# Kernel tuning notes

Measured on AMD Instinct MI355X. Metric: run time of the kernel, lower is better.

## Reference

```python
import jax, jax.numpy as jnp
import numpy as np

D = 100  # input_size


def _gru_scan(x, h0, wi, wh, bi, bh):
    # x: [B,T,Din], h0: [B,H], wi: [3H,Din], wh: [3H,H]  (PyTorch r,z,n gate order)
    xw = jnp.einsum('btd,gd->btg', x, wi) + bi  # [B,T,3H]
    def step(h, xt):
        gh = h @ wh.T + bh
        xr, xz, xn = jnp.split(xt, 3, axis=-1)
        hr, hz, hn = jnp.split(gh, 3, axis=-1)
        r = jax.nn.sigmoid(xr + hr)
        z = jax.nn.sigmoid(xz + hz)
        n = jnp.tanh(xn + r * hn)
        hn2 = (1 - z) * n + z * h
        return hn2, hn2
    _, ys = jax.lax.scan(step, h0, jnp.swapaxes(xw, 0, 1))
    return jnp.swapaxes(ys, 0, 1)  # [B,T,H]


def _bigru(x, wi, wh, bi, bh):
    B = x.shape[0]
    H = wh.shape[-1]
    h0 = jnp.zeros((B, H), x.dtype)
    f = _gru_scan(x, h0, wi[0], wh[0], bi[0], bh[0])
    b = _gru_scan(x[:, ::-1], h0, wi[1], wh[1], bi[1], bh[1])[:, ::-1]
    return jnp.concatenate([f, b], axis=-1)


def _gru_cell(x, h, wi, wh, bi, bh):
    gx = x @ wi.T + bi
    gh = h @ wh.T + bh
    xr, xz, xn = jnp.split(gx, 3, axis=-1)
    hr, hz, hn = jnp.split(gh, 3, axis=-1)
    r = jax.nn.sigmoid(xr + hr)
    z = jax.nn.sigmoid(xz + hz)
    n = jnp.tanh(xn + r * hn)
    return (1 - z) * n + z * h


def setup_inputs() -> dict:
    key = jax.random.key(0)
    ks = iter(jax.random.split(key, 40))
    def n(shape, s=0.08):
        return (jax.random.normal(next(ks), shape) * s).astype(jnp.float32)
    B, T, L, V = 32, 512, 64, 400000
    inp = {
        'x_word': jax.random.randint(next(ks), (B, T), 0, V),
        'x_query': jax.random.randint(next(ks), (B, L), 0, V),
        'embed': n((V, D), 0.3),
        'ctx_wi': n((2, 3 * D, D)), 'ctx_wh': n((2, 3 * D, D)),
        'ctx_bi': n((2, 3 * D)), 'ctx_bh': n((2, 3 * D)),
        'mod0_wi': n((2, 3 * D, 8 * D)), 'mod0_wh': n((2, 3 * D, D)),
        'mod0_bi': n((2, 3 * D)), 'mod0_bh': n((2, 3 * D)),
        'mod1_wi': n((2, 3 * D, 2 * D)), 'mod1_wh': n((2, 3 * D, D)),
        'mod1_bi': n((2, 3 * D)), 'mod1_bh': n((2, 3 * D)),
        'w_sim': n((6 * D,)),
        'enc_wi': n((12 * D, 2 * D)), 'enc_wh': n((12 * D, 4 * D)),
        'enc_bi': n((12 * D,)), 'enc_bh': n((12 * D,)),
        'dec_wi': n((12 * D, 2 * D)), 'dec_wh': n((12 * D, 4 * D)),
        'dec_bi': n((12 * D,)), 'dec_bh': n((12 * D,)),
        'w1': n((2 * D, 4 * D)), 'w2': n((2 * D, 4 * D)), 'vt': n((2 * D,)),
    }
    return inp


def reference(x_word, x_query, embed, ctx_wi, ctx_wh, ctx_bi, ctx_bh,
              mod0_wi, mod0_wh, mod0_bi, mod0_bh, mod1_wi, mod1_wh, mod1_bi, mod1_bh,
              w_sim, enc_wi, enc_wh, enc_bi, enc_bh, dec_wi, dec_wh, dec_bi, dec_bh,
              w1, w2, vt):
    B, T = x_word.shape
    # shared bidirectional context encoder over both context and query
    h = _bigru(embed[x_word], ctx_wi, ctx_wh, ctx_bi, ctx_bh)   # [B,T,2D]
    u = _bigru(embed[x_query], ctx_wi, ctx_wh, ctx_bi, ctx_bh)  # [B,L,2D]
    # trilinear similarity W @ cat(h,u,h*u), fused (no [B,T,L,6D] materialization)
    w1s, w2s, w3s = jnp.split(w_sim, 3)
    S = (jnp.einsum('btd,d->bt', h, w1s)[:, :, None]
         + jnp.einsum('bld,d->bl', u, w2s)[:, None, :]
         + jnp.einsum('btd,bld->btl', h * w3s, u))               # [B,T,L]
    c2q = jnp.einsum('btl,bld->btd', jax.nn.softmax(S, axis=-1), u)
    b_att = jax.nn.softmax(jnp.max(S, axis=2), axis=-1)          # [B,T]
    q2c = jnp.einsum('bt,btd->bd', b_att, h)[:, None, :]         # [B,1,2D]
    G = jnp.concatenate([h, c2q, h * c2q, h * q2c], axis=-1)     # [B,T,8D]
    # 2-layer bidirectional modeling GRU
    M = _bigru(G, mod0_wi, mod0_wh, mod0_bi, mod0_bh)
    M = _bigru(M, mod1_wi, mod1_wh, mod1_bi, mod1_bh)            # [B,T,2D]
    # pointer network
    enc = _gru_scan(M, jnp.zeros((B, 4 * D), M.dtype), enc_wi, enc_wh, enc_bi, enc_bh)  # [B,T,4D]
    enc_w1 = jnp.einsum('bth,ph->btp', enc, w1)                  # precompute W1 @ enc
    hid = jnp.zeros((B, 4 * D), M.dtype)
    dec_in = jnp.zeros((B, 2 * D), M.dtype)  # never updated (as in original)
    probs = []
    for _ in range(2):  # answers = 2 (start, end)
        hid = _gru_cell(dec_in, hid, dec_wi, dec_wh, dec_bi, dec_bh)
        blend = jnp.tanh(enc_w1 + (hid @ w2.T)[:, None, :])      # [B,T,2D]
        out = jnp.einsum('btp,p->bt', blend, vt)
        probs.append(jax.nn.log_softmax(out, axis=-1))
    return jnp.stack(probs, axis=1)  # [B,2,T]
```

## Files before the change

kernel.cpp:

```cpp
#include <hip/hip_runtime.h>
#include <hip/hip_bf16.h>

typedef __hip_bfloat16 bf16;
typedef unsigned long long u64;
typedef __attribute__((ext_vector_type(8))) short s8v;
typedef __attribute__((ext_vector_type(4))) short s4v;
typedef __attribute__((ext_vector_type(4))) float f4v;

#define DEV __device__ __forceinline__

DEV float to_f32(float x) { return x; }
DEV float to_f32(bf16 x) { return __bfloat162float(x); }
DEV void store_c(float* p, float v) { *p = v; }
DEV void store_c(bf16* p, float v) { *p = __float2bfloat16(v); }
DEV float sigmf(float x) { return 1.f / (1.f + __expf(-x)); }

__global__ void gather_embed_bf(const int* __restrict__ idx, const float* __restrict__ embed,
                                bf16* __restrict__ out, int ntok) {
  int i = blockIdx.x * blockDim.x + threadIdx.x;
  if (i >= ntok * 100) return;
  int t = i / 100;
  int d = i - t * 100;
  out[i] = __float2bfloat16(embed[(size_t)idx[t] * 100 + d]);
}

__global__ void cvt_bf16(const float* __restrict__ in, bf16* __restrict__ out, int n) {
  int i = blockIdx.x * blockDim.x + threadIdx.x;
  if (i < n) out[i] = __float2bfloat16(in[i]);
}

template <typename TC, bool HAS_BIAS>
__global__ __launch_bounds__(256) void gemm_mfma(
    const bf16* __restrict__ A, const bf16* __restrict__ W,
    const float* __restrict__ bias, TC* __restrict__ C,
    int M, int N, int K) {
  __shared__ short Als[128 * 32];
  __shared__ short Wls[64 * 32];
  const int tid = threadIdx.x;
  const int m0 = blockIdx.x * 128;
  const int n0 = blockIdx.y * 64;
  const int lane = tid & 63;
  const int wv = tid >> 6;
  const int wm = wv >> 1, wn = wv & 1;
  const int lq = lane >> 4, lr = lane & 15;
  const int arow = tid >> 1;
  const int ah = tid & 1;
  const int wrow = (tid & 127) >> 1;

  f4v acc[4][2];
#pragma unroll
  for (int i = 0; i < 4; ++i)
#pragma unroll
    for (int j = 0; j < 2; ++j) acc[i][j] = (f4v){0.f, 0.f, 0.f, 0.f};

  for (int k0 = 0; k0 < K; k0 += 32) {
#pragma unroll
    for (int ss = 0; ss < 2; ++ss) {
      int s = 2 * ah + ss;
      int kk = k0 + s * 8;
      short* dst = &Als[arow * 32 + s * 8];
      const short* src = (const short*)(A + (size_t)(m0 + arow) * K + kk);
      if (kk + 8 <= K) {
        *(s4v*)dst = *(const s4v*)src;
        *(s4v*)(dst + 4) = *(const s4v*)(src + 4);
      } else {
#pragma unroll
        for (int j = 0; j < 8; ++j) dst[j] = (kk + j < K) ? src[j] : (short)0;
      }
    }
    if (tid < 128) {
      int nrow = n0 + wrow;
#pragma unroll
      for (int ss = 0; ss < 2; ++ss) {
        int s = 2 * (tid & 1) + ss;
        int kk = k0 + s * 8;
        short* dst = &Wls[wrow * 32 + s * 8];
        if (nrow < N) {
          const short* src = (const short*)(W + (size_t)nrow * K + kk);
          if (kk + 8 <= K) {
            *(s4v*)dst = *(const s4v*)src;
            *(s4v*)(dst + 4) = *(const s4v*)(src + 4);
          } else {
#pragma unroll
            for (int j = 0; j < 8; ++j) dst[j] = (kk + j < K) ? src[j] : (short)0;
          }
        } else {
#pragma unroll
          for (int j = 0; j < 8; ++j) dst[j] = (short)0;
        }
      }
    }
    __syncthreads();
    s8v af[4], bfr[2];
#pragma unroll
    for (int mi = 0; mi < 4; ++mi) {
      int r = wm * 64 + mi * 16 + lr;
      af[mi] = *(const s8v*)&Als[r * 32 + lq * 8];
    }
#pragma unroll
    for (int ni = 0; ni < 2; ++ni) {
      int r = wn * 32 + ni * 16 + lr;
      bfr[ni] = *(const s8v*)&Wls[r * 32 + lq * 8];
    }
#pragma unroll
    for (int mi = 0; mi < 4; ++mi)
#pragma unroll
      for (int ni = 0; ni < 2; ++ni)
        acc[mi][ni] = __builtin_amdgcn_mfma_f32_16x16x32_bf16(af[mi], bfr[ni], acc[mi][ni], 0, 0, 0);
    __syncthreads();
  }
#pragma unroll
  for (int mi = 0; mi < 4; ++mi) {
#pragma unroll
    for (int ni = 0; ni < 2; ++ni) {
      int n = n0 + wn * 32 + ni * 16 + lr;
      if (n >= N) continue;
      float bv = HAS_BIAS ? bias[n] : 0.f;
#pragma unroll
      for (int r = 0; r < 4; ++r) {
        int m = m0 + wm * 64 + mi * 16 + lq * 4 + r;
        store_c(&C[(size_t)m * N + n], acc[mi][ni][r] + bv);
      }
    }
  }
}

template <typename TO>
__global__ __launch_bounds__(320) void gru_scan100_reg(
    const bf16* __restrict__ xw_f, const bf16* __restrict__ xw_b,
    const float* __restrict__ wh,
    const float* __restrict__ bh,
    TO* __restrict__ out,
    int T) {
  const int b = blockIdx.x, dir = blockIdx.y;
  const bf16* xw = dir ? xw_b : xw_f;
  __shared__ float h_s[100];
  __shared__ float g_s[300];
  const int tid = threadIdx.x;
  float w[100];
  float bias = 0.f;
  if (tid < 300) {
    const float* wrow = wh + (size_t)dir * 30000 + (size_t)tid * 100;
#pragma unroll
    for (int c = 0; c < 25; ++c) {
      float4 v = *(const float4*)(wrow + 4 * c);
      w[4 * c] = v.x; w[4 * c + 1] = v.y; w[4 * c + 2] = v.z; w[4 * c + 3] = v.w;
    }
    bias = bh[dir * 300 + tid];
  }
  if (tid < 100) h_s[tid] = 0.f;
  __syncthreads();
  for (int step = 0; step < T; ++step) {
    int t = dir ? (T - 1 - step) : step;
    if (tid < 300) {
      float a0 = bias, a1 = 0.f, a2 = 0.f, a3 = 0.f;
#pragma unroll
      for (int c = 0; c < 25; ++c) {
        float4 h4 = *(const float4*)(&h_s[4 * c]);
        a0 += w[4 * c] * h4.x; a1 += w[4 * c + 1] * h4.y;
        a2 += w[4 * c + 2] * h4.z; a3 += w[4 * c + 3] * h4.w;
      }
      g_s[tid] = (a0 + a1) + (a2 + a3);
    }
    __syncthreads();
    if (tid < 100) {
      size_t base = ((size_t)b * T + t) * 300;
      float xr = to_f32(xw[base + tid]);
      float xz = to_f32(xw[base + 100 + tid]);
      float xn = to_f32(xw[base + 200 + tid]);
      float rr = sigmf(xr + g_s[tid]);
      float zz = sigmf(xz + g_s[100 + tid]);
      float nn = tanhf(xn + rr * g_s[200 + tid]);
      float hn = (1.f - zz) * nn + zz * h_s[tid];
      h_s[tid] = hn;
      store_c(&out[((size_t)b * T + t) * 200 + dir * 100 + tid], hn);
    }
    __syncthreads();
  }
}

__global__ __launch_bounds__(640) void gru_scan_enc_tag(
    const bf16* __restrict__ xw,
    const float* __restrict__ wh,
    const float* __restrict__ bh,
    bf16* __restrict__ out,
    u64* __restrict__ hx,
    int T) {
  const int b = blockIdx.x, s = blockIdx.y;
  __shared__ float h_s[400];
  __shared__ float g_s[150];
  const int tid = threadIdx.x;
  const int g = tid >> 2, p = tid & 3;
  const bool active = (tid < 600);
  float w[100];
  float bias = 0.f;
  if (active) {
    int i = g % 50, grp = g / 50;
    int gidx = grp * 400 + s * 50 + i;
    const float* wrow = wh + (size_t)gidx * 400 + p * 100;
#pragma unroll
    for (int c = 0; c < 25; ++c) {
      float4 v = *(const float4*)(wrow + 4 * c);
      w[4 * c] = v.x; w[4 * c + 1] = v.y; w[4 * c + 2] = v.z; w[4 * c + 3] = v.w;
    }
    if (p == 0) bias = bh[gidx];
  }
  for (int k = tid; k < 400; k += 640) h_s[k] = 0.f;
  const int myi = s * 50 + tid;
  float pxr = 0.f, pxz = 0.f, pxn = 0.f;
  if (tid < 50) {
    size_t base0 = (size_t)b * T * 1200;
    pxr = to_f32(xw[base0 + myi]);
    pxz = to_f32(xw[base0 + 400 + myi]);
    pxn = to_f32(xw[base0 + 800 + myi]);
  }
  __syncthreads();

  for (int t = 0; t < T; ++t) {
    if (active) {
      float a0 = bias, a1 = 0.f, a2 = 0.f, a3 = 0.f;
      const int hb = p * 100;
#pragma unroll
      for (int c = 0; c < 25; ++c) {
        float4 h4 = *(const float4*)(&h_s[hb + 4 * c]);
        a0 += w[4 * c] * h4.x; a1 += w[4 * c + 1] * h4.y;
        a2 += w[4 * c + 2] * h4.z; a3 += w[4 * c + 3] * h4.w;
      }
      float acc = (a0 + a1) + (a2 + a3);
      acc += __shfl_xor(acc, 1);
      acc += __shfl_xor(acc, 2);
      if (p == 0) g_s[g] = acc;
    }
    __syncthreads();
    const int par = (t + 1) & 1;
    u64* hxp = hx + ((size_t)b * 2 + par) * 400;
    if (tid < 50) {
      float rr = sigmf(pxr + g_s[tid]);
      float zz = sigmf(pxz + g_s[50 + tid]);
      float nn = tanhf(pxn + rr * g_s[100 + tid]);
      float hn = (1.f - zz) * nn + zz * h_s[myi];
      out[((size_t)b * T + t) * 400 + myi] = __float2bfloat16(hn);
      h_s[myi] = hn;
      u64 pack = (u64)__float_as_uint(hn) | ((u64)(unsigned)(t + 1) << 32);
      __hip_atomic_store(&hxp[myi], pack, __ATOMIC_RELAXED, __HIP_MEMORY_SCOPE_AGENT);
      if (t + 1 < T) {
        size_t basen = ((size_t)b * T + (t + 1)) * 1200;
        pxr = to_f32(xw[basen + myi]);
        pxz = to_f32(xw[basen + 400 + myi]);
        pxn = to_f32(xw[basen + 800 + myi]);
      }
    }
    if (tid < 400 && (tid / 50) != s) {
      const u64* src = &hxp[tid];
      u64 v;
      for (;;) {
        v = __hip_atomic_load(src, __ATOMIC_RELAXED, __HIP_MEMORY_SCOPE_AGENT);
        if ((unsigned)(v >> 32) == (unsigned)(t + 1)) break;
        __builtin_amdgcn_s_sleep(1);
      }
      h_s[tid] = __uint_as_float((unsigned)v);
    }
    __syncthreads();
  }
}

__global__ __launch_bounds__(64) void rowdot200(const float* __restrict__ X, const float* __restrict__ w,
                                                float* __restrict__ out, int rows) {
  int r = blockIdx.x;
  int lane = threadIdx.x;
  const float* x = X + (size_t)r * 200;
  float s = x[lane] * w[lane] + x[lane + 64] * w[lane + 64] + x[lane + 128] * w[lane + 128];
  if (lane < 8) s += x[lane + 192] * w[lane + 192];
  for (int off = 32; off; off >>= 1) s += __shfl_down(s, off);
  if (lane == 0) out[r] = s;
}

__global__ __launch_bounds__(256) void attn_main(
    const float* __restrict__ h,
    const float* __restrict__ u,
    const float* __restrict__ th,
    const float* __restrict__ tu,
    const float* __restrict__ w_sim,
    float* __restrict__ c2q,
    float* __restrict__ smax,
    int T) {
  const int b = blockIdx.x;
  const int t0 = blockIdx.y * 32;
  __shared__ float u_s[64 * 201];
  __shared__ float tu_s[64];
  __shared__ float w3_s[200];
  __shared__ float hw3_s[200];
  __shared__ float Sp[4][64];
  __shared__ float A_s[64];
  const int tid = threadIdx.x;
  for (int i = tid; i < 64 * 200; i += 256) {
    int l = i / 200, d = i - l * 200;
    u_s[l * 201 + d] = u[((size_t)b * 64 + l) * 200 + d];
  }
  if (tid < 64) tu_s[tid] = tu[b * 64 + tid];
  if (tid < 200) w3_s[tid] = w_sim[400 + tid];
  __syncthreads();
  for (int tt = 0; tt < 32; ++tt) {
    int t = t0 + tt;
    if (tid < 200) hw3_s[tid] = h[((size_t)b * T + t) * 200 + tid] * w3_s[tid];
    __syncthreads();
    int l = tid & 63, q = tid >> 6;
    float p = 0.f;
    for (int d = q * 50; d < q * 50 + 50; ++d) p += hw3_s[d] * u_s[l * 201 + d];
    Sp[q][l] = p;
    __syncthreads();
    if (tid < 64) {
      float s = th[b * T + t] + tu_s[l] + Sp[0][l] + Sp[1][l] + Sp[2][l] + Sp[3][l];
      float m = s;
      for (int off = 32; off; off >>= 1) m = fmaxf(m, __shfl_xor(m, off));
      float e = __expf(s - m);
      float ssum = e;
      for (int off = 32; off; off >>= 1) ssum += __shfl_xor(ssum, off);
      A_s[l] = e / ssum;
      if (l == 0) smax[b * T + t] = m;
    }
    __syncthreads();
    if (tid < 200) {
      float acc = 0.f;
      for (int l2 = 0; l2 < 64; ++l2) acc += A_s[l2] * u_s[l2 * 201 + tid];
      c2q[((size_t)b * T + t) * 200 + tid] = acc;
    }
    __syncthreads();
  }
}

__global__ __launch_bounds__(256) void softmax_T(const float* __restrict__ in, float* __restrict__ outv, int T) {
  int b = blockIdx.x;
  int tid = threadIdx.x;
  __shared__ float red[256];
  float m = -1e30f;
  for (int t = tid; t < T; t += 256) m = fmaxf(m, in[b * T + t]);
  red[tid] = m;
  __syncthreads();
  for (int s = 128; s; s >>= 1) {
    if (tid < s) red[tid] = fmaxf(red[tid], red[tid + s]);
    __syncthreads();
  }
  m = red[0];
  __syncthreads();
  float sum = 0.f;
  for (int t = tid; t < T; t += 256) sum += __expf(in[b * T + t] - m);
  red[tid] = sum;
  __syncthreads();
  for (int s = 128; s; s >>= 1) {
    if (tid < s) red[tid] += red[tid + s];
    __syncthreads();
  }
  float inv = 1.f / red[0];
  for (int t = tid; t < T; t += 256) outv[b * T + t] = __expf(in[b * T + t] - m) * inv;
}

__global__ __launch_bounds__(256) void q2c_kernel(const float* __restrict__ batt, const float* __restrict__ h,
                                                  float* __restrict__ q2c, int T) {
  int b = blockIdx.x;
  int tid = threadIdx.x;
  if (tid < 200) {
    float acc = 0.f;
    for (int t = 0; t < T; ++t) acc += batt[b * T + t] * h[((size_t)b * T + t) * 200 + tid];
    q2c[b * 200 + tid] = acc;
  }
}

__global__ void build_G(const float* __restrict__ h, const float* __restrict__ c2q,
                        const float* __restrict__ q2c, bf16* __restrict__ G, int T) {
  size_t i = (size_t)blockIdx.x * blockDim.x + threadIdx.x;
  if (i >= (size_t)32 * T * 200) return;
  size_t row = i / 200;
  int d = (int)(i - row * 200);
  int b = (int)(row / T);
  float hv = h[i];
  float cv = c2q[i];
  float qv = q2c[b * 200 + d];
  bf16* g = G + row * 800;
  g[d] = __float2bfloat16(hv);
  g[200 + d] = __float2bfloat16(cv);
  g[400 + d] = __float2bfloat16(hv * cv);
  g[600 + d] = __float2bfloat16(hv * qv);
}

__global__ __launch_bounds__(512) void decoder_small(
    const float* __restrict__ dwh,
    const float* __restrict__ dbi, const float* __restrict__ dbh,
    const float* __restrict__ w2,
    float* __restrict__ d2out) {
  __shared__ float hid[400];
  __shared__ float hid2[400];
  __shared__ float gh[1200];
  const int tid = threadIdx.x;
  if (tid < 400) {
    float r = sigmf(dbi[tid] + dbh[tid]);
    float z = sigmf(dbi[400 + tid] + dbh[400 + tid]);
    float n = tanhf(dbi[800 + tid] + r * dbh[800 + tid]);
    hid[tid] = (1.f - z) * n;
  }
  __syncthreads();
  if (tid < 200) {
    float a = 0.f;
    for (int k = 0; k < 400; ++k) a += w2[(size_t)tid * 400 + k] * hid[k];
    d2out[tid] = a;
  }
  for (int j = tid; j < 1200; j += 512) {
    float a = dbh[j];
    for (int k = 0; k < 400; ++k) a += dwh[(size_t)j * 400 + k] * hid[k];
    gh[j] = a;
  }
  __syncthreads();
  if (tid < 400) {
    float r = sigmf(dbi[tid] + gh[tid]);
    float z = sigmf(dbi[400 + tid] + gh[400 + tid]);
    float n = tanhf(dbi[800 + tid] + r * gh[800 + tid]);
    hid2[tid] = (1.f - z) * n + z * hid[tid];
  }
  __syncthreads();
  if (tid < 200) {
    float a = 0.f;
    for (int k = 0; k < 400; ++k) a += w2[(size_t)tid * 400 + k] * hid2[k];
    d2out[200 + tid] = a;
  }
}

__global__ __launch_bounds__(64) void logits_kernel(
    const float* __restrict__ encw1,
    const float* __restrict__ d2,
    const float* __restrict__ vt,
    float* __restrict__ outp,
    int T) {
  int row = blockIdx.x;
  int b = row / T, t = row - b * T;
  int lane = threadIdx.x;
  const float* e = encw1 + (size_t)row * 200;
  float s0 = 0.f, s1 = 0.f;
  for (int p = lane; p < 200; p += 64) {
    float ev = e[p], v = vt[p];
    s0 += tanhf(ev + d2[p]) * v;
    s1 += tanhf(ev + d2[200 + p]) * v;
  }
  for (int off = 32; off; off >>= 1) {
    s0 += __shfl_down(s0, off);
    s1 += __shfl_down(s1, off);
  }
  if (lane == 0) {
    outp[((size_t)b * 2 + 0) * T + t] = s0;
    outp[((size_t)b * 2 + 1) * T + t] = s1;
  }
}

__global__ __launch_bounds__(256) void log_softmax_T(float* __restrict__ x, int T) {
  int row = blockIdx.x;
  float* p = x + (size_t)row * T;
  __shared__ float red[256];
  int tid = threadIdx.x;
  float m = -1e30f;
  for (int t = tid; t < T; t += 256) m = fmaxf(m, p[t]);
  red[tid] = m;
  __syncthreads();
  for (int s = 128; s; s >>= 1) {
    if (tid < s) red[tid] = fmaxf(red[tid], red[tid + s]);
    __syncthreads();
  }
  m = red[0];
  __syncthreads();
  float sum = 0.f;
  for (int t = tid; t < T; t += 256) sum += __expf(p[t] - m);
  red[tid] = sum;
  __syncthreads();
  for (int s = 128; s; s >>= 1) {
    if (tid < s) red[tid] += red[tid + s];
    __syncthreads();
  }
  float lse = m + __logf(red[0]);
  __syncthreads();
  for (int t = tid; t < T; t += 256) p[t] = p[t] - lse;
}

extern "C" void kernel_launch(void* const* d_in, const int* in_sizes, int n_in,
                              void* d_out, int out_size, void* d_ws, size_t ws_size,
                              hipStream_t stream) {
  (void)in_sizes; (void)n_in; (void)out_size; (void)ws_size;
  const int B = 32, T = 512, L = 64;
  const int BT = B * T;
  const int BL = B * L;

  const int* x_word = (const int*)d_in[0];
  const int* x_query = (const int*)d_in[1];
  const float* embed = (const float*)d_in[2];
  const float* ctx_wi = (const float*)d_in[3];
  const float* ctx_wh = (const float*)d_in[4];
  const float* ctx_bi = (const float*)d_in[5];
  const float* ctx_bh = (const float*)d_in[6];
  const float* mod0_wi = (const float*)d_in[7];
  const float* mod0_wh = (const float*)d_in[8];
  const float* mod0_bi = (const float*)d_in[9];
  const float* mod0_bh = (const float*)d_in[10];
  const float* mod1_wi = (const float*)d_in[11];
  const float* mod1_wh = (const float*)d_in[12];
  const float* mod1_bi = (const float*)d_in[13];
  const float* mod1_bh = (const float*)d_in[14];
  const float* w_sim = (const float*)d_in[15];
  const float* enc_wi = (const float*)d_in[16];
  const float* enc_wh = (const float*)d_in[17];
  const float* enc_bi = (const float*)d_in[18];
  const float* enc_bh = (const float*)d_in[19];
  const float* dec_wh = (const float*)d_in[21];
  const float* dec_bi = (const float*)d_in[22];
  const float* dec_bh = (const float*)d_in[23];
  const float* w1 = (const float*)d_in[24];
  const float* w2 = (const float*)d_in[25];
  const float* vt = (const float*)d_in[26];
  float* out_f = (float*)d_out;

  char* ws = (char*)d_ws;
  size_t off = 0;
  auto alloc = [&](size_t bytes) -> void* {
    void* p = ws + off;
    off += (bytes + 255) & ~(size_t)255;
    return p;
  };
  u64* hx = (u64*)alloc((size_t)B * 2 * 400 * 8);
  bf16* ewbf = (bf16*)alloc((size_t)BT * 100 * 2);
  bf16* eqbf = (bf16*)alloc((size_t)BL * 100 * 2);
  bf16* ctx_wibf = (bf16*)alloc((size_t)60000 * 2);
  bf16* mod0_wibf = (bf16*)alloc((size_t)480000 * 2);
  bf16* mod1_wibf = (bf16*)alloc((size_t)120000 * 2);
  bf16* enc_wibf = (bf16*)alloc((size_t)240000 * 2);
  bf16* w1bf = (bf16*)alloc((size_t)80000 * 2);
  char* RA = (char*)alloc((size_t)BT * 1200 * 2);
  bf16* xwA = (bf16*)RA;
  bf16* xwB = (bf16*)(RA + (size_t)BT * 300 * 2);
  bf16* xwe = (bf16*)RA;
  bf16* xwqF = (bf16*)alloc((size_t)BL * 300 * 2);
  bf16* xwqB = (bf16*)alloc((size_t)BL * 300 * 2);
  char* RB = (char*)alloc((size_t)BT * 800 * 2);
  bf16* G = (bf16*)RB;
  bf16* enc_outbf = (bf16*)RB;
  char* RC = (char*)alloc((size_t)2 * BT * 200 * 4);
  float* h_cat = (float*)RC;
  float* c2q = (float*)(RC + (size_t)BT * 200 * 4);
  bf16* M0bf = (bf16*)c2q;
  bf16* Mxbf = (bf16*)h_cat;
  float* encw1 = c2q;
  float* u_cat = (float*)alloc((size_t)BL * 200 * 4);
  float* th = (float*)alloc((size_t)BT * 4);
  float* tu = (float*)alloc((size_t)BL * 4);
  float* smaxb = (float*)alloc((size_t)BT * 4);
  float* batt = (float*)alloc((size_t)BT * 4);
  float* q2cb = (float*)alloc((size_t)B * 200 * 4);
  float* d2 = (float*)alloc((size_t)400 * 4);

  hipMemsetAsync(hx, 0, (size_t)B * 2 * 400 * 8, stream);

  cvt_bf16<<<(60000 + 255) / 256, 256, 0, stream>>>(ctx_wi, ctx_wibf, 60000);
  cvt_bf16<<<(480000 + 255) / 256, 256, 0, stream>>>(mod0_wi, mod0_wibf, 480000);
  cvt_bf16<<<(120000 + 255) / 256, 256, 0, stream>>>(mod1_wi, mod1_wibf, 120000);
  cvt_bf16<<<(240000 + 255) / 256, 256, 0, stream>>>(enc_wi, enc_wibf, 240000);
  cvt_bf16<<<(80000 + 255) / 256, 256, 0, stream>>>(w1, w1bf, 80000);
  gather_embed_bf<<<(BT * 100 + 255) / 256, 256, 0, stream>>>(x_word, embed, ewbf, BT);
  gather_embed_bf<<<(BL * 100 + 255) / 256, 256, 0, stream>>>(x_query, embed, eqbf, BL);

  {
    dim3 g(BT / 128, (300 + 63) / 64);
    gemm_mfma<bf16, true><<<g, 256, 0, stream>>>(ewbf, ctx_wibf, ctx_bi, xwA, BT, 300, 100);
    gemm_mfma<bf16, true><<<g, 256, 0, stream>>>(ewbf, ctx_wibf + 30000, ctx_bi + 300, xwB, BT, 300, 100);
    dim3 gq(BL / 128, (300 + 63) / 64);
    gemm_mfma<bf16, true><<<gq, 256, 0, stream>>>(eqbf, ctx_wibf, ctx_bi, xwqF, BL, 300, 100);
    gemm_mfma<bf16, true><<<gq, 256, 0, stream>>>(eqbf, ctx_wibf + 30000, ctx_bi + 300, xwqB, BL, 300, 100);
  }

  gru_scan100_reg<float><<<dim3(B, 2), 320, 0, stream>>>(xwA, xwB, ctx_wh, ctx_bh, h_cat, T);
  gru_scan100_reg<float><<<dim3(B, 2), 320, 0, stream>>>(xwqF, xwqB, ctx_wh, ctx_bh, u_cat, L);

  rowdot200<<<BT, 64, 0, stream>>>(h_cat, w_sim, th, BT);
  rowdot200<<<BL, 64, 0, stream>>>(u_cat, w_sim + 200, tu, BL);
  attn_main<<<dim3(B, T / 32), 256, 0, stream>>>(h_cat, u_cat, th, tu, w_sim, c2q, smaxb, T);
  softmax_T<<<B, 256, 0, stream>>>(smaxb, batt, T);
  q2c_kernel<<<B, 256, 0, stream>>>(batt, h_cat, q2cb, T);
  build_G<<<(BT * 200 + 255) / 256, 256, 0, stream>>>(h_cat, c2q, q2cb, G, T);

  {
    dim3 g(BT / 128, (300 + 63) / 64);
    gemm_mfma<bf16, true><<<g, 256, 0, stream>>>(G, mod0_wibf, mod0_bi, xwA, BT, 300, 800);
    gemm_mfma<bf16, true><<<g, 256, 0, stream>>>(G, mod0_wibf + 240000, mod0_bi + 300, xwB, BT, 300, 800);
  }
  gru_scan100_reg<bf16><<<dim3(B, 2), 320, 0, stream>>>(xwA, xwB, mod0_wh, mod0_bh, M0bf, T);

  {
    dim3 g(BT / 128, (300 + 63) / 64);
    gemm_mfma<bf16, true><<<g, 256, 0, stream>>>(M0bf, mod1_wibf, mod1_bi, xwA, BT, 300, 200);
    gemm_mfma<bf16, true><<<g, 256, 0, stream>>>(M0bf, mod1_wibf + 60000, mod1_bi + 300, xwB, BT, 300, 200);
  }
  gru_scan100_reg<bf16><<<dim3(B, 2), 320, 0, stream>>>(xwA, xwB, mod1_wh, mod1_bh, Mxbf, T);

  {
    dim3 g(BT / 128, (1200 + 63) / 64);
    gemm_mfma<bf16, true><<<g, 256, 0, stream>>>(Mxbf, enc_wibf, enc_bi, xwe, BT, 1200, 200);
  }
  gru_scan_enc_tag<<<dim3(B, 8), 640, 0, stream>>>(xwe, enc_wh, enc_bh, enc_outbf, hx, T);
  {
    dim3 g(BT / 128, (200 + 63) / 64);
    gemm_mfma<float, false><<<g, 256, 0, stream>>>(enc_outbf, w1bf, nullptr, encw1, BT, 200, 400);
  }

  decoder_small<<<1, 512, 0, stream>>>(dec_wh, dec_bi, dec_bh, w2, d2);
  logits_kernel<<<BT, 64, 0, stream>>>(encw1, d2, vt, out_f, T);
  log_softmax_T<<<B * 2, 256, 0, stream>>>(out_f, T);
}
```

Measured before the change: 3.580 ms.

## Fuse small kernels, merge fwd/bwd input GEMMs, prefetch GRU gate inputs

Merges the five weight-conversion launches into one kernel, and merges the forward and backward input-projection GEMMs into a single N=600 GEMM with an interleaved per-timestep layout. The rowdot kernels are folded into attn_main and softmax is fused with q2c. The GRU scans now prefetch the next timestep's gate inputs during the current step and batch the shared-memory h loads ahead of the FMA loop. This is meant to cut launch count and serial latency in the recurrent loop, at the cost of more register use and some redundant rowdot work per attention block.

Measured after the change: 3.340 ms. -6.7%, faster.

```diff
diff --git a/kernel.cpp b/kernel.cpp
--- a/kernel.cpp
+++ b/kernel.cpp
@@ -24,9 +24,21 @@
   out[i] = __float2bfloat16(embed[(size_t)idx[t] * 100 + d]);
 }
 
-__global__ void cvt_bf16(const float* __restrict__ in, bf16* __restrict__ out, int n) {
+__global__ void cvt_all(const float* __restrict__ s0, bf16* __restrict__ d0,
+                        const float* __restrict__ s1, bf16* __restrict__ d1,
+                        const float* __restrict__ s2, bf16* __restrict__ d2,
+                        const float* __restrict__ s3, bf16* __restrict__ d3,
+                        const float* __restrict__ s4, bf16* __restrict__ d4) {
   int i = blockIdx.x * blockDim.x + threadIdx.x;
-  if (i < n) out[i] = __float2bfloat16(in[i]);
+  if (i < 60000) d0[i] = __float2bfloat16(s0[i]);
+  i -= 60000;
+  if (i >= 0 && i < 480000) d1[i] = __float2bfloat16(s1[i]);
+  i -= 480000;
+  if (i >= 0 && i < 120000) d2[i] = __float2bfloat16(s2[i]);
+  i -= 120000;
+  if (i >= 0 && i < 240000) d3[i] = __float2bfloat16(s3[i]);
+  i -= 240000;
+  if (i >= 0 && i < 80000) d4[i] = __float2bfloat16(s4[i]);
 }
 
 template <typename TC, bool HAS_BIAS>
@@ -127,13 +139,12 @@
 
 template <typename TO>
 __global__ __launch_bounds__(320) void gru_scan100_reg(
-    const bf16* __restrict__ xw_f, const bf16* __restrict__ xw_b,
+    const bf16* __restrict__ xw,
     const float* __restrict__ wh,
     const float* __restrict__ bh,
     TO* __restrict__ out,
     int T) {
   const int b = blockIdx.x, dir = blockIdx.y;
-  const bf16* xw = dir ? xw_b : xw_f;
   __shared__ float h_s[100];
   __shared__ float g_s[300];
   const int tid = threadIdx.x;
@@ -149,31 +160,44 @@
     bias = bh[dir * 300 + tid];
   }
   if (tid < 100) h_s[tid] = 0.f;
+  float pxr = 0.f, pxz = 0.f, pxn = 0.f;
+  if (tid < 100) {
+    int t0 = dir ? (T - 1) : 0;
+    size_t base = ((size_t)b * T + t0) * 600 + dir * 300;
+    pxr = to_f32(xw[base + tid]);
+    pxz = to_f32(xw[base + 100 + tid]);
+    pxn = to_f32(xw[base + 200 + tid]);
+  }
   __syncthreads();
   for (int step = 0; step < T; ++step) {
     int t = dir ? (T - 1 - step) : step;
     if (tid < 300) {
+      float4 hbuf[25];
+#pragma unroll
+      for (int c = 0; c < 25; ++c) hbuf[c] = *(const float4*)(&h_s[4 * c]);
       float a0 = bias, a1 = 0.f, a2 = 0.f, a3 = 0.f;
 #pragma unroll
       for (int c = 0; c < 25; ++c) {
-        float4 h4 = *(const float4*)(&h_s[4 * c]);
-        a0 += w[4 * c] * h4.x; a1 += w[4 * c + 1] * h4.y;
-        a2 += w[4 * c + 2] * h4.z; a3 += w[4 * c + 3] * h4.w;
+        a0 += w[4 * c] * hbuf[c].x; a1 += w[4 * c + 1] * hbuf[c].y;
+        a2 += w[4 * c + 2] * hbuf[c].z; a3 += w[4 * c + 3] * hbuf[c].w;
       }
       g_s[tid] = (a0 + a1) + (a2 + a3);
     }
     __syncthreads();
     if (tid < 100) {
-      size_t base = ((size_t)b * T + t) * 300;
-      float xr = to_f32(xw[base + tid]);
-      float xz = to_f32(xw[base + 100 + tid]);
-      float xn = to_f32(xw[base + 200 + tid]);
-      float rr = sigmf(xr + g_s[tid]);
-      float zz = sigmf(xz + g_s[100 + tid]);
-      float nn = tanhf(xn + rr * g_s[200 + tid]);
+      float rr = sigmf(pxr + g_s[tid]);
+      float zz = sigmf(pxz + g_s[100 + tid]);
+      float nn = tanhf(pxn + rr * g_s[200 + tid]);
       float hn = (1.f - zz) * nn + zz * h_s[tid];
       h_s[tid] = hn;
       store_c(&out[((size_t)b * T + t) * 200 + dir * 100 + tid], hn);
+      if (step + 1 < T) {
+        int tn = dir ? (T - 2 - step) : (step + 1);
+        size_t basen = ((size_t)b * T + tn) * 600 + dir * 300;
+        pxr = to_f32(xw[basen + tid]);
+        pxz = to_f32(xw[basen + 100 + tid]);
+        pxn = to_f32(xw[basen + 200 + tid]);
+      }
     }
     __syncthreads();
   }
@@ -218,13 +242,15 @@
 
   for (int t = 0; t < T; ++t) {
     if (active) {
+      const int hb = p * 100;
+      float4 hbuf[25];
+#pragma unroll
+      for (int c = 0; c < 25; ++c) hbuf[c] = *(const float4*)(&h_s[hb + 4 * c]);
       float a0 = bias, a1 = 0.f, a2 = 0.f, a3 = 0.f;
-      const int hb = p * 100;
 #pragma unroll
       for (int c = 0; c < 25; ++c) {
-        float4 h4 = *(const float4*)(&h_s[hb + 4 * c]);
-        a0 += w[4 * c] * h4.x; a1 += w[4 * c + 1] * h4.y;
-        a2 += w[4 * c + 2] * h4.z; a3 += w[4 * c + 3] * h4.w;
+        a0 += w[4 * c] * hbuf[c].x; a1 += w[4 * c + 1] * hbuf[c].y;
+        a2 += w[4 * c + 2] * hbuf[c].z; a3 += w[4 * c + 3] * hbuf[c].w;
       }
       float acc = (a0 + a1) + (a2 + a3);
       acc += __shfl_xor(acc, 1);
@@ -264,22 +290,9 @@
   }
 }
 
-__global__ __launch_bounds__(64) void rowdot200(const float* __restrict__ X, const float* __restrict__ w,
-                                                float* __restrict__ out, int rows) {
-  int r = blockIdx.x;
-  int lane = threadIdx.x;
-  const float* x = X + (size_t)r * 200;
-  float s = x[lane] * w[lane] + x[lane + 64] * w[lane + 64] + x[lane + 128] * w[lane + 128];
-  if (lane < 8) s += x[lane + 192] * w[lane + 192];
-  for (int off = 32; off; off >>= 1) s += __shfl_down(s, off);
-  if (lane == 0) out[r] = s;
-}
-
 __global__ __launch_bounds__(256) void attn_main(
     const float* __restrict__ h,
     const float* __restrict__ u,
-    const float* __restrict__ th,
-    const float* __restrict__ tu,
     const float* __restrict__ w_sim,
     float* __restrict__ c2q,
     float* __restrict__ smax,
@@ -287,8 +300,8 @@
   const int b = blockIdx.x;
   const int t0 = blockIdx.y * 32;
   __shared__ float u_s[64 * 201];
-  __shared__ float tu_s[64];
-  __shared__ float w3_s[200];
+  __shared__ float w1_s[200], w2_s[200], w3_s[200];
+  __shared__ float th_s[32], tu_s[64];
   __shared__ float hw3_s[200];
   __shared__ float Sp[4][64];
   __shared__ float A_s[64];
@@ -297,8 +310,30 @@
     int l = i / 200, d = i - l * 200;
     u_s[l * 201 + d] = u[((size_t)b * 64 + l) * 200 + d];
   }
-  if (tid < 64) tu_s[tid] = tu[b * 64 + tid];
-  if (tid < 200) w3_s[tid] = w_sim[400 + tid];
+  if (tid < 200) {
+    w1_s[tid] = w_sim[tid];
+    w2_s[tid] = w_sim[200 + tid];
+    w3_s[tid] = w_sim[400 + tid];
+  }
+  __syncthreads();
+  {
+    int r = tid >> 2, sg = tid & 3;
+    float p = 0.f;
+    for (int j = 0; j < 50; ++j) p += u_s[r * 201 + sg * 50 + j] * w2_s[sg * 50 + j];
+    p += __shfl_down(p, 2);
+    p += __shfl_down(p, 1);
+    if (sg == 0) tu_s[r] = p;
+  }
+  {
+    int r = tid >> 3, sg = tid & 7;
+    float p = 0.f;
+    const float* hr = h + ((size_t)b * T + t0 + r) * 200 + sg * 25;
+    for (int j = 0; j < 25; ++j) p += hr[j] * w1_s[sg * 25 + j];
+    p += __shfl_down(p, 4);
+    p += __shfl_down(p, 2);
+    p += __shfl_down(p, 1);
+    if (sg == 0) th_s[r] = p;
+  }
   __syncthreads();
   for (int tt = 0; tt < 32; ++tt) {
     int t = t0 + tt;
@@ -310,7 +345,7 @@
     Sp[q][l] = p;
     __syncthreads();
     if (tid < 64) {
-      float s = th[b * T + t] + tu_s[l] + Sp[0][l] + Sp[1][l] + Sp[2][l] + Sp[3][l];
+      float s = th_s[tt] + tu_s[l] + Sp[0][l] + Sp[1][l] + Sp[2][l] + Sp[3][l];
       float m = s;
       for (int off = 32; off; off >>= 1) m = fmaxf(m, __shfl_xor(m, off));
       float e = __expf(s - m);
@@ -329,12 +364,15 @@
   }
 }
 
-__global__ __launch_bounds__(256) void softmax_T(const float* __restrict__ in, float* __restrict__ outv, int T) {
+__global__ __launch_bounds__(256) void softmax_q2c(
+    const float* __restrict__ smaxv, const float* __restrict__ h,
+    float* __restrict__ q2c, int T) {
   int b = blockIdx.x;
   int tid = threadIdx.x;
   __shared__ float red[256];
+  __shared__ float batt_s[512];
   float m = -1e30f;
-  for (int t = tid; t < T; t += 256) m = fmaxf(m, in[b * T + t]);
+  for (int t = tid; t < T; t += 256) m = fmaxf(m, smaxv[b * T + t]);
   red[tid] = m;
   __syncthreads();
   for (int s = 128; s; s >>= 1) {
@@ -344,7 +382,11 @@
   m = red[0];
   __syncthreads();
   float sum = 0.f;
-  for (int t = tid; t < T; t += 256) sum += __expf(in[b * T + t] - m);
+  for (int t = tid; t < T; t += 256) {
+    float e = __expf(smaxv[b * T + t] - m);
+    batt_s[t] = e;
+    sum += e;
+  }
   red[tid] = sum;
   __syncthreads();
   for (int s = 128; s; s >>= 1) {
@@ -352,17 +394,11 @@
     __syncthreads();
   }
   float inv = 1.f / red[0];
-  for (int t = tid; t < T; t += 256) outv[b * T + t] = __expf(in[b * T + t] - m) * inv;
-}
-
-__global__ __launch_bounds__(256) void q2c_kernel(const float* __restrict__ batt, const float* __restrict__ h,
-                                                  float* __restrict__ q2c, int T) {
-  int b = blockIdx.x;
-  int tid = threadIdx.x;
+  __syncthreads();
   if (tid < 200) {
     float acc = 0.f;
-    for (int t = 0; t < T; ++t) acc += batt[b * T + t] * h[((size_t)b * T + t) * 200 + tid];
-    q2c[b * 200 + tid] = acc;
+    for (int t = 0; t < T; ++t) acc += batt_s[t] * h[((size_t)b * T + t) * 200 + tid];
+    q2c[b * 200 + tid] = acc * inv;
   }
 }
 
@@ -384,9 +420,8 @@
 }
 
 __global__ __launch_bounds__(512) void decoder_small(
-    const float* __restrict__ dwh,
-    const float* __restrict__ dbi, const float* __restrict__ dbh,
-    const float* __restrict__ w2,
+    const float* __restrict__ dwh, const float* __restrict__ dbi,
+    const float* __restrict__ dbh, const float* __restrict__ w2,
     float* __restrict__ d2out) {
   __shared__ float hid[400];
   __shared__ float hid2[400];
@@ -425,11 +460,8 @@
 }
 
 __global__ __launch_bounds__(64) void logits_kernel(
-    const float* __restrict__ encw1,
-    const float* __restrict__ d2,
-    const float* __restrict__ vt,
-    float* __restrict__ outp,
-    int T) {
+    const float* __restrict__ encw1, const float* __restrict__ d2,
+    const float* __restrict__ vt, float* __restrict__ outp, int T) {
   int row = blockIdx.x;
   int b = row / T, t = row - b * T;
   int lane = threadIdx.x;
@@ -530,11 +562,9 @@
   bf16* enc_wibf = (bf16*)alloc((size_t)240000 * 2);
   bf16* w1bf = (bf16*)alloc((size_t)80000 * 2);
   char* RA = (char*)alloc((size_t)BT * 1200 * 2);
-  bf16* xwA = (bf16*)RA;
-  bf16* xwB = (bf16*)(RA + (size_t)BT * 300 * 2);
+  bf16* xwFB = (bf16*)RA;
   bf16* xwe = (bf16*)RA;
-  bf16* xwqF = (bf16*)alloc((size_t)BL * 300 * 2);
-  bf16* xwqB = (bf16*)alloc((size_t)BL * 300 * 2);
+  bf16* xwq = (bf16*)alloc((size_t)BL * 600 * 2);
   char* RB = (char*)alloc((size_t)BT * 800 * 2);
   bf16* G = (bf16*)RB;
   bf16* enc_outbf = (bf16*)RB;
@@ -545,65 +575,37 @@
   bf16* Mxbf = (bf16*)h_cat;
   float* encw1 = c2q;
   float* u_cat = (float*)alloc((size_t)BL * 200 * 4);
-  float* th = (float*)alloc((size_t)BT * 4);
-  float* tu = (float*)alloc((size_t)BL * 4);
   float* smaxb = (float*)alloc((size_t)BT * 4);
-  float* batt = (float*)alloc((size_t)BT * 4);
   float* q2cb = (float*)alloc((size_t)B * 200 * 4);
   float* d2 = (float*)alloc((size_t)400 * 4);
 
   hipMemsetAsync(hx, 0, (size_t)B * 2 * 400 * 8, stream);
 
-  cvt_bf16<<<(60000 + 255) / 256, 256, 0, stream>>>(ctx_wi, ctx_wibf, 60000);
-  cvt_bf16<<<(480000 + 255) / 256, 256, 0, stream>>>(mod0_wi, mod0_wibf, 480000);
-  cvt_bf16<<<(120000 + 255) / 256, 256, 0, stream>>>(mod1_wi, mod1_wibf, 120000);
-  cvt_bf16<<<(240000 + 255) / 256, 256, 0, stream>>>(enc_wi, enc_wibf, 240000);
-  cvt_bf16<<<(80000 + 255) / 256, 256, 0, stream>>>(w1, w1bf, 80000);
+  cvt_all<<<(980000 + 255) / 256, 256, 0, stream>>>(ctx_wi, ctx_wibf, mod0_wi, mod0_wibf,
+                                                    mod1_wi, mod1_wibf, enc_wi, enc_wibf,
+                                                    w1, w1bf);
   gather_embed_bf<<<(BT * 100 + 255) / 256, 256, 0, stream>>>(x_word, embed, ewbf, BT);
   gather_embed_bf<<<(BL * 100 + 255) / 256, 256, 0, stream>>>(x_query, embed, eqbf, BL);
 
-  {
-    dim3 g(BT / 128, (300 + 63) / 64);
-    gemm_mfma<bf16, true><<<g, 256, 0, stream>>>(ewbf, ctx_wibf, ctx_bi, xwA, BT, 300, 100);
-    gemm_mfma<bf16, true><<<g, 256, 0, stream>>>(ewbf, ctx_wibf + 30000, ctx_bi + 300, xwB, BT, 300, 100);
-    dim3 gq(BL / 128, (300 + 63) / 64);
-    gemm_mfma<bf16, true><<<gq, 256, 0, stream>>>(eqbf, ctx_wibf, ctx_bi, xwqF, BL, 300, 100);
-    gemm_mfma<bf16, true><<<gq, 256, 0, stream>>>(eqbf, ctx_wibf + 30000, ctx_bi + 300, xwqB, BL, 300, 100);
-  }
-
-  gru_scan100_reg<float><<<dim3(B, 2), 320, 0, stream>>>(xwA, xwB, ctx_wh, ctx_bh, h_cat, T);
-  gru_scan100_reg<float><<<dim3(B, 2), 320, 0, stream>>>(xwqF, xwqB, ctx_wh, ctx_bh, u_cat, L);
-
-  rowdot200<<<BT, 64, 0, stream>>>(h_cat, w_sim, th, BT);
-  rowdot200<<<BL, 64, 0, stream>>>(u_cat, w_sim + 200, tu, BL);
-  attn_main<<<dim3(B, T / 32), 256, 0, stream>>>(h_cat, u_cat, th, tu, w_sim, c2q, smaxb, T);
-  softmax_T<<<B, 256, 0, stream>>>(smaxb, batt, T);
-  q2c_kernel<<<B, 256, 0, stream>>>(batt, h_cat, q2cb, T);
+  gemm_mfma<bf16, true><<<dim3(BT / 128, 10), 256, 0, stream>>>(ewbf, ctx_wibf, ctx_bi, xwFB, BT, 600, 100);
+  gemm_mfma<bf16, true><<<dim3(BL / 128, 10), 256, 0, stream>>>(eqbf, ctx_wibf, ctx_bi, xwq, BL, 600, 100);
+
+  gru_scan100_reg<float><<<dim3(B, 2), 320, 0, stream>>>(xwFB, ctx_wh, ctx_bh, h_cat, T);
+  gru_scan100_reg<float><<<dim3(B, 2), 320, 0, stream>>>(xwq, ctx_wh, ctx_bh, u_cat, L);
+
+  attn_main<<<dim3(B, T / 32), 256, 0, stream>>>(h_cat, u_cat, w_sim, c2q, smaxb, T);
+  softmax_q2c<<<B, 256, 0, stream>>>(smaxb, h_cat, q2cb, T);
   build_G<<<(BT * 200 + 255) / 256, 256, 0, stream>>>(h_cat, c2q, q2cb, G, T);
 
-  {
-    dim3 g(BT / 128, (300 + 63) / 64);
-    gemm_mfma<bf16, true><<<g, 256, 0, stream>>>(G, mod0_wibf, mod0_bi, xwA, BT, 300, 800);
-    gemm_mfma<bf16, true><<<g, 256, 0, stream>>>(G, mod0_wibf + 240000, mod0_bi + 300, xwB, BT, 300, 800);
-  }
-  gru_scan100_reg<bf16><<<dim3(B, 2), 320, 0, stream>>>(xwA, xwB, mod0_wh, mod0_bh, M0bf, T);
-
-  {
-    dim3 g(BT / 128, (300 + 63) / 64);
-    gemm_mfma<bf16, true><<<g, 256, 0, stream>>>(M0bf, mod1_wibf, mod1_bi, xwA, BT, 300, 200);
-    gemm_mfma<bf16, true><<<g, 256, 0, stream>>>(M0bf, mod1_wibf + 60000, mod1_bi + 300, xwB, BT, 300, 200);
-  }
-  gru_scan100_reg<bf16><<<dim3(B, 2), 320, 0, stream>>>(xwA, xwB, mod1_wh, mod1_bh, Mxbf, T);
-
-  {
-    dim3 g(BT / 128, (1200 + 63) / 64);
-    gemm_mfma<bf16, true><<<g, 256, 0, stream>>>(Mxbf, enc_wibf, enc_bi, xwe, BT, 1200, 200);
-  }
+  gemm_mfma<bf16, true><<<dim3(BT / 128, 10), 256, 0, stream>>>(G, mod0_wibf, mod0_bi, xwFB, BT, 600, 800);
+  gru_scan100_reg<bf16><<<dim3(B, 2), 320, 0, stream>>>(xwFB, mod0_wh, mod0_bh, M0bf, T);
+
+  gemm_mfma<bf16, true><<<dim3(BT / 128, 10), 256, 0, stream>>>(M0bf, mod1_wibf, mod1_bi, xwFB, BT, 600, 200);
+  gru_scan100_reg<bf16><<<dim3(B, 2), 320, 0, stream>>>(xwFB, mod1_wh, mod1_bh, Mxbf, T);
+
+  gemm_mfma<bf16, true><<<dim3(BT / 128, (1200 + 63) / 64), 256, 0, stream>>>(Mxbf, enc_wibf, enc_bi, xwe, BT, 1200, 200);
   gru_scan_enc_tag<<<dim3(B, 8), 640, 0, stream>>>(xwe, enc_wh, enc_bh, enc_outbf, hx, T);
-  {
-    dim3 g(BT / 128, (200 + 63) / 64);
-    gemm_mfma<float, false><<<g, 256, 0, stream>>>(enc_outbf, w1bf, nullptr, encw1, BT, 200, 400);
-  }
+  gemm_mfma<float, false><<<dim3(BT / 128, (200 + 63) / 64), 256, 0, stream>>>(enc_outbf, w1bf, nullptr, encw1, BT, 200, 400);
 
   decoder_small<<<1, 512, 0, stream>>>(dec_wh, dec_bi, dec_bh, w2, d2);
   logits_kernel<<<BT, 64, 0, stream>>>(encw1, d2, vt, out_f, T);
```
